# Optimization experiments

Measured on AMD Instinct MI355X. Metric: run time of the kernel, lower is better.

The kernel has to match this reference:

```python
import jax, jax.numpy as jnp
import numpy as np

DN = ('NHWC', 'HWIO', 'NHWC')
ITERS, LAM, MU = 100, 0.005, 1.0


def _psf_matrix():
    # Gaussian PSF mapping a 72x72 hi-res grid onto a 9x9 camera image -> (5184, 81)
    hi = (np.arange(72) + 0.5) * 9.0 / 72.0   # hi-res positions in lo-res pixel units
    lo = np.arange(9) + 0.5                   # lo-res pixel centers
    sig = 1.5                                 # sigma/px_size = 150/100
    g = np.exp(-(hi[:, None] - lo[None, :]) ** 2 / (2.0 * sig * sig))  # (72, 9)
    mat = np.einsum('ai,bj->abij', g, g).reshape(5184, 81)
    mat /= np.linalg.norm(mat, 2)  # spectral-normalize so the 1/mu gradient step converges
    return mat.astype(np.float32)


def _conv(x, w, b=None, stride=1, padding='VALID'):
    y = jax.lax.conv_general_dilated(x, w, (stride, stride), padding, dimension_numbers=DN)
    return y if b is None else y + b


def _convT(x, w):
    return jax.lax.conv_transpose(x, w, (3, 3), 'SAME', dimension_numbers=DN)


def _bn(x, g, b, eps=1e-3):
    m = jnp.mean(x, axis=(0, 1, 2), keepdims=True)
    v = jnp.var(x, axis=(0, 1, 2), keepdims=True)
    return g * (x - m) * jax.lax.rsqrt(v + eps) + b


def _maxpool(x, k):
    return jax.lax.reduce_window(x, -jnp.inf, jax.lax.max, (1, k, k, 1), (1, k, k, 1), 'SAME')


def _fista(x, mat):
    # x: (B,9,9,3) -> per-channel flatten (B,81,3); sparse code y: (B,5184,3)
    B = x.shape[0]
    im = x.reshape(B, 81, 3)
    y0 = jnp.zeros((B, 5184, 3), x.dtype)
    thr = LAM / MU

    def step(carry, _):
        y_tmp, y_last, t = carry
        proj = jnp.einsum('sm,bsc->bmc', mat, y_tmp)          # mat^T @ y
        re = jnp.einsum('sm,bmc->bsc', mat, im - proj)        # mat @ (im - mat^T y)
        w = y_tmp + re / MU
        y_new = jax.nn.relu(w - thr) - jax.nn.relu(-w - thr)  # soft threshold
        t_n = (1.0 + jnp.sqrt(1.0 + 4.0 * t * t)) / 2.0
        y_mom = y_new + (t - 1.0) / t_n * (y_new - y_last)    # momentum
        return (y_mom, y_new, t_n), None

    (_, y_final, _), _ = jax.lax.scan(step, (y0, y0, jnp.float32(1.0)), None, length=ITERS)
    return y_final  # (B, 5184, 3)


def _forward(x, mat, bn_x_g, bn_x_b, w5, b5, wx2, bx2, wy1, by1, wy7, by7,
             bn_y_g, bn_y_b, ww1, bw1, wd1, bnd1_g, bnd1_b, wd2, bnd2_g, bnd2_b,
             wu1, bnu1_g, bnu1_b, wu2):
    B = x.shape[0]
    # --- x path: compressed sensing -> inception conv branch ---
    xi = _fista(x, mat).reshape(B, 72, 72, 3)
    xi = jnp.pad(xi, ((0, 0), (1, 0), (1, 0), (0, 0)), mode='reflect')  # (B,73,73,3)
    xi = _bn(xi, bn_x_g, bn_x_b)
    xi = _conv(xi, w5, b5)                 # valid 5x5 -> (B,69,69,8)
    xi = _maxpool(xi, 4)                   # -> (B,18,18,8)
    xi = jax.nn.relu(_conv(xi, wx2, bx2))  # 1x1 -> (B,18,18,2)
    xi = _maxpool(xi, 2)                   # -> (B,9,9,2)
    # --- y path ---
    yi = jax.nn.relu(_conv(x, wy1, by1))
    yi = _conv(yi, wy7, by7, padding='SAME')
    yi = _bn(yi, bn_y_g, bn_y_b)           # (B,9,9,1)
    # --- w path ---
    wi = jax.nn.relu(_conv(x, ww1, bw1))   # (B,9,9,1)
    # --- z path: small U-net ---
    z1 = jax.nn.leaky_relu(_bn(_conv(x, wd1, stride=3, padding='SAME'), bnd1_g, bnd1_b), 0.2)   # (B,3,3,12)
    z2 = jax.nn.leaky_relu(_bn(_conv(z1, wd2, stride=3, padding='SAME'), bnd2_g, bnd2_b), 0.2)  # (B,1,1,24)
    z = jax.nn.relu(_bn(_convT(z2, wu1), bnu1_g, bnu1_b))  # (B,3,3,12)
    z = jnp.concatenate([z, z1], axis=-1)                  # (B,3,3,24)
    z = jax.nn.relu(_convT(z, wu2))                        # (B,9,9,1)
    return jnp.concatenate([wi, xi, yi, z], axis=-1)       # (B,9,9,5)


def setup_inputs() -> dict:
    key = jax.random.key(0)
    ks = jax.random.split(key, 12)
    n = jax.random.normal
    B = 64
    return {
        'x': jax.random.uniform(ks[0], (B, 9, 9, 3), jnp.float32),
        'mat': jnp.asarray(_psf_matrix()),
        'bn_x_g': jnp.ones(3), 'bn_x_b': jnp.zeros(3),
        'w5': n(ks[1], (5, 5, 3, 8)) * 0.1, 'b5': jnp.zeros(8),
        'wx2': n(ks[2], (1, 1, 8, 2)) * 0.1, 'bx2': jnp.zeros(2),
        'wy1': n(ks[3], (1, 1, 3, 1)) * 0.1, 'by1': jnp.zeros(1),
        'wy7': n(ks[4], (7, 7, 1, 1)) * 0.1, 'by7': jnp.zeros(1),
        'bn_y_g': jnp.ones(1), 'bn_y_b': jnp.zeros(1),
        'ww1': n(ks[5], (1, 1, 3, 1)) * 0.1, 'bw1': jnp.zeros(1),
        'wd1': n(ks[6], (3, 3, 3, 12)) * 0.1, 'bnd1_g': jnp.ones(12), 'bnd1_b': jnp.zeros(12),
        'wd2': n(ks[7], (3, 3, 12, 24)) * 0.1, 'bnd2_g': jnp.ones(24), 'bnd2_b': jnp.zeros(24),
        'wu1': n(ks[8], (3, 3, 24, 12)) * 0.1, 'bnu1_g': jnp.ones(12), 'bnu1_b': jnp.zeros(12),
        'wu2': n(ks[9], (3, 3, 24, 1)) * 0.1,
    }


def reference(x, mat, bn_x_g, bn_x_b, w5, b5, wx2, bx2, wy1, by1, wy7, by7,
              bn_y_g, bn_y_b, ww1, bw1, wd1, bnd1_g, bnd1_b, wd2, bnd2_g, bnd2_b,
              wu1, bnu1_g, bnu1_b, wu2):
    return _forward(x, mat, bn_x_g, bn_x_b, w5, b5, wx2, bx2, wy1, by1, wy7, by7,
                    bn_y_g, bn_y_b, ww1, bw1, wd1, bnd1_g, bnd1_b, wd2, bnd2_g, bnd2_b,
                    wu1, bnu1_g, bnu1_b, wu2)
```

## Files before the change

kernel.cpp:

```cpp
#include <hip/hip_runtime.h>
#include <hip/hip_bf16.h>
#include <math.h>

#define NS 5184

__device__ __forceinline__ float dpp_xor1_add(float v) {
  int s = __builtin_amdgcn_update_dpp(0, __float_as_int(v), 0xB1, 0xF, 0xF, true);
  return v + __int_as_float(s);
}
__device__ __forceinline__ float dpp_xor2_add(float v) {
  int s = __builtin_amdgcn_update_dpp(0, __float_as_int(v), 0x4E, 0xF, 0xF, true);
  return v + __int_as_float(s);
}

__global__ __launch_bounds__(576, 3) void cs_fista_small(
    const float* __restrict__ x, const float* __restrict__ mat,
    const float* __restrict__ wy1, const float* __restrict__ by1,
    const float* __restrict__ wy7, const float* __restrict__ by7,
    const float* __restrict__ bn_y_g, const float* __restrict__ bn_y_b,
    const float* __restrict__ ww1, const float* __restrict__ bw1,
    const float* __restrict__ wd1, const float* __restrict__ bnd1_g, const float* __restrict__ bnd1_b,
    const float* __restrict__ wd2, const float* __restrict__ bnd2_g, const float* __restrict__ bnd2_b,
    const float* __restrict__ wu1, const float* __restrict__ bnu1_g, const float* __restrict__ bnu1_b,
    const float* __restrict__ wu2,
    float* __restrict__ ws_y, float* __restrict__ bns, float* __restrict__ out)
{
  __shared__ __align__(16) float smem[16384];
  const int tid = threadIdx.x;
  const int blk = blockIdx.x;

  if (blk < 192) {
    const int bb = blk / 3, ch = blk % 3;
    float* GT  = smem;
    float* W1T = smem + 684;
    float* M9T = smem + 1368;
    float* IM  = smem + 1476;
    float* RED = smem + 1560;

    const int a    = tid >> 3;
    const int slot = tid & 7;
    const int b0   = slot * 9;

    for (int k = tid; k < 648; k += 576) {
      int aa = k / 9, i = k % 9;
      GT[i*76 + aa] = sqrtf(mat[aa*5913 + i*10]);
    }
    if (tid < 81) IM[tid] = x[(bb*81 + tid)*3 + ch];
    __syncthreads();

    float g_blk[9][9], g_row[9], gim[9];
    #pragma unroll
    for (int bl = 0; bl < 9; ++bl)
      #pragma unroll
      for (int j = 0; j < 9; ++j)
        g_blk[bl][j] = GT[j*76 + b0 + bl];
    #pragma unroll
    for (int i = 0; i < 9; ++i) g_row[i] = GT[i*76 + a];
    #pragma unroll
    for (int j = 0; j < 9; ++j) {
      float acc = 0.f;
      #pragma unroll
      for (int i = 0; i < 9; ++i) acc = fmaf(g_row[i], IM[i*9 + j], acc);
      gim[j] = acc;
    }
    float ym[9], yl[9];
    #pragma unroll
    for (int bl = 0; bl < 9; ++bl) { ym[bl] = 0.f; yl[bl] = 0.f; }
    const int lbase = (tid & 63) & 56;

    float t = 1.f;
    for (int it = 0; it < 100; ++it) {
      float pj[9];
      #pragma unroll
      for (int j = 0; j < 9; ++j) {
        float acc = 0.f;
        #pragma unroll
        for (int bl = 0; bl < 9; ++bl) acc = fmaf(ym[bl], g_blk[bl][j], acc);
        pj[j] = acc;
      }
      #pragma unroll
      for (int j = 0; j < 9; ++j) {
        pj[j] = dpp_xor1_add(pj[j]);
        pj[j] = dpp_xor2_add(pj[j]);
        pj[j] += __shfl_xor(pj[j], 4);
      }
      float sel = pj[0];
      sel = (slot == 1) ? pj[1] : sel;
      sel = (slot == 2) ? pj[2] : sel;
      sel = (slot == 3) ? pj[3] : sel;
      sel = (slot == 4) ? pj[4] : sel;
      sel = (slot == 5) ? pj[5] : sel;
      sel = (slot == 6) ? pj[6] : sel;
      sel = (slot == 7) ? pj[7] : sel;
      W1T[slot*76 + a] = sel;
      if (slot == 0) W1T[8*76 + a] = pj[8];
      __syncthreads();
      if (tid < 324) {
        int o = tid >> 2, sg = tid & 3;
        int i = o / 9, j = o - i*9;
        const float* gb = GT  + i*76;
        const float* wb = W1T + j*76;
        const float4* gr = (const float4*)(gb + sg*16);
        const float4* wr = (const float4*)(wb + sg*16);
        float4 g0 = gr[0], w0 = wr[0];
        float4 g1 = gr[1], w1 = wr[1];
        float4 g2 = gr[2], w2 = wr[2];
        float4 g3 = gr[3], w3 = wr[3];
        float p0 = g0.x*w0.x, p1 = g0.y*w0.y, p2 = g0.z*w0.z, p3 = g0.w*w0.w;
        p0 = fmaf(g1.x, w1.x, p0); p1 = fmaf(g1.y, w1.y, p1);
        p2 = fmaf(g1.z, w1.z, p2); p3 = fmaf(g1.w, w1.w, p3);
        p0 = fmaf(g2.x, w2.x, p0); p1 = fmaf(g2.y, w2.y, p1);
        p2 = fmaf(g2.z, w2.z, p2); p3 = fmaf(g2.w, w2.w, p3);
        p0 = fmaf(g3.x, w3.x, p0); p1 = fmaf(g3.y, w3.y, p1);
        p2 = fmaf(g3.z, w3.z, p2); p3 = fmaf(g3.w, w3.w, p3);
        if (sg == 0) {
          const float4* gt = (const float4*)(gb + 64);
          const float4* wt = (const float4*)(wb + 64);
          float4 g4 = gt[0], w4 = wt[0];
          float4 g5 = gt[1], w5 = wt[1];
          p0 = fmaf(g4.x, w4.x, p0); p1 = fmaf(g4.y, w4.y, p1);
          p2 = fmaf(g4.z, w4.z, p2); p3 = fmaf(g4.w, w4.w, p3);
          p0 = fmaf(g5.x, w5.x, p0); p1 = fmaf(g5.y, w5.y, p1);
          p2 = fmaf(g5.z, w5.z, p2); p3 = fmaf(g5.w, w5.w, p3);
        }
        float acc = (p0 + p1) + (p2 + p3);
        acc = dpp_xor1_add(acc);
        acc = dpp_xor2_add(acc);
        if (sg == 0) M9T[j*12 + i] = acc;
      }
      __syncthreads();
      const float tn  = 0.5f * (1.f + sqrtf(1.f + 4.f*t*t));
      const float mom = (t - 1.f) / tn;
      float gsel = gim[0];
      gsel = (slot == 1) ? gim[1] : gsel;
      gsel = (slot == 2) ? gim[2] : gsel;
      gsel = (slot == 3) ? gim[3] : gsel;
      gsel = (slot == 4) ? gim[4] : gsel;
      gsel = (slot == 5) ? gim[5] : gsel;
      gsel = (slot == 6) ? gim[6] : gsel;
      gsel = (slot == 7) ? gim[7] : gsel;
      float4 c0 = *(const float4*)(M9T + slot*12);
      float4 c1 = *(const float4*)(M9T + slot*12 + 4);
      float  c8 = M9T[slot*12 + 8];
      float tjs = gsel;
      tjs = fmaf(-g_row[0], c0.x, tjs);
      tjs = fmaf(-g_row[1], c0.y, tjs);
      tjs = fmaf(-g_row[2], c0.z, tjs);
      tjs = fmaf(-g_row[3], c0.w, tjs);
      tjs = fmaf(-g_row[4], c1.x, tjs);
      tjs = fmaf(-g_row[5], c1.y, tjs);
      tjs = fmaf(-g_row[6], c1.z, tjs);
      tjs = fmaf(-g_row[7], c1.w, tjs);
      tjs = fmaf(-g_row[8], c8,   tjs);
      float tj8 = 0.f;
      if (slot == 7) {
        float4 d0 = *(const float4*)(M9T + 96);
        float4 d1 = *(const float4*)(M9T + 100);
        float  d8 = M9T[104];
        tj8 = gim[8];
        tj8 = fmaf(-g_row[0], d0.x, tj8);
        tj8 = fmaf(-g_row[1], d0.y, tj8);
        tj8 = fmaf(-g_row[2], d0.z, tj8);
        tj8 = fmaf(-g_row[3], d0.w, tj8);
        tj8 = fmaf(-g_row[4], d1.x, tj8);
        tj8 = fmaf(-g_row[5], d1.y, tj8);
        tj8 = fmaf(-g_row[6], d1.z, tj8);
        tj8 = fmaf(-g_row[7], d1.w, tj8);
        tj8 = fmaf(-g_row[8], d8,   tj8);
      }
      float t2[9];
      t2[0] = __shfl(tjs, lbase + 0);
      t2[1] = __shfl(tjs, lbase + 1);
      t2[2] = __shfl(tjs, lbase + 2);
      t2[3] = __shfl(tjs, lbase + 3);
      t2[4] = __shfl(tjs, lbase + 4);
      t2[5] = __shfl(tjs, lbase + 5);
      t2[6] = __shfl(tjs, lbase + 6);
      t2[7] = __shfl(tjs, lbase + 7);
      t2[8] = __shfl(tj8, lbase + 7);
      #pragma unroll
      for (int bl = 0; bl < 9; ++bl) {
        float re = 0.f;
        #pragma unroll
        for (int j = 0; j < 9; ++j) re = fmaf(t2[j], g_blk[bl][j], re);
        float w  = ym[bl] + re;
        float yn = fmaxf(w - 0.005f, 0.f) - fmaxf(-w - 0.005f, 0.f);
        float y2 = fmaf(mom, yn - yl[bl], yn);
        yl[bl] = yn;
        ym[bl] = y2;
      }
      t = tn;
    }
    float* wp = ws_y + (bb*3 + ch)*NS + a*72 + b0;
    float wsum = 0.f, wss = 0.f;
    #pragma unroll
    for (int bl = 0; bl < 9; ++bl) {
      wp[bl] = yl[bl];
      float wt = (float)((1 + (a == 1)) * (1 + (b0 + bl == 1)));
      wsum = fmaf(wt, yl[bl], wsum);
      wss  = fmaf(wt * yl[bl], yl[bl], wss);
    }
    #pragma unroll
    for (int off = 32; off > 0; off >>= 1) {
      wsum += __shfl_down(wsum, off);
      wss  += __shfl_down(wss, off);
    }
    __syncthreads();
    if ((tid & 63) == 0) { RED[tid >> 6] = wsum; RED[16 + (tid >> 6)] = wss; }
    __syncthreads();
    if (tid == 0) {
      float s = 0.f, s2 = 0.f;
      for (int w = 0; w < 9; ++w) { s += RED[w]; s2 += RED[16 + w]; }
      atomicAdd(&bns[ch],     s);
      atomicAdd(&bns[3 + ch], s2);
    }
  } else {
    float* TY  = smem;
    float* Y7  = smem + 5184;
    float* Z1  = smem;
    float* Z2  = smem + 6912;
    float* ZU  = smem + 8448;
    float* RED = smem + 15360;

    const float vwy10 = wy1[0], vwy11 = wy1[1], vwy12 = wy1[2], vby1 = by1[0];
    const float vww10 = ww1[0], vww11 = ww1[1], vww12 = ww1[2], vbw1 = bw1[0];
    for (int k = tid; k < NS; k += 576) {
      const float* xp = x + 3*k;
      float x0 = xp[0], x1 = xp[1], x2 = xp[2];
      out[5*k] = fmaxf(fmaf(x2, vww12, fmaf(x1, vww11, fmaf(x0, vww10, vbw1))), 0.f);
      TY[k]    = fmaxf(fmaf(x2, vwy12, fmaf(x1, vwy11, fmaf(x0, vwy10, vby1))), 0.f);
    }
    __syncthreads();
    float ps = 0.f, pss = 0.f;
    const float vby7 = by7[0];
    for (int k = tid; k < NS; k += 576) {
      int bb = k / 81, p = k % 81, h = p / 9, w = p % 9;
      float acc = vby7;
      for (int kh = 0; kh < 7; ++kh) {
        int hh = h + kh - 3;
        if (hh < 0 || hh > 8) continue;
        for (int kw = 0; kw < 7; ++kw) {
          int wi = w + kw - 3;
          if (wi < 0 || wi > 8) continue;
          acc = fmaf(TY[bb*81 + hh*9 + wi], wy7[kh*7 + kw], acc);
        }
      }
      Y7[k] = acc;
      ps += acc; pss += acc*acc;
    }
    #pragma unroll
    for (int off = 32; off > 0; off >>= 1) {
      ps  += __shfl_down(ps, off);
      pss += __shfl_down(pss, off);
    }
    if ((tid & 63) == 0) { RED[tid >> 6] = ps; RED[16 + (tid >> 6)] = pss; }
    __syncthreads();
    if (tid == 0) {
      float s = 0.f, s2 = 0.f;
      for (int w = 0; w < 9; ++w) { s += RED[w]; s2 += RED[16 + w]; }
      float m  = s  * (1.f/5184.f);
      float v  = s2 * (1.f/5184.f) - m*m;
      float sc = bn_y_g[0] * rsqrtf(v + 1e-3f);
      RED[32] = sc;
      RED[33] = bn_y_b[0] - m*sc;
    }
    __syncthreads();
    {
      float sc = RED[32], sh = RED[33];
      for (int k = tid; k < NS; k += 576) out[5*k + 3] = fmaf(Y7[k], sc, sh);
    }
    __syncthreads();
    if (tid < 128) RED[tid] = 0.f;
    __syncthreads();
    for (int k = tid; k < 6912; k += 576) {
      int bb = k / 108, r = k % 108, u = r / 36, v3 = (r / 12) % 3, oc = r % 12;
      float acc = 0.f;
      #pragma unroll
      for (int kh = 0; kh < 3; ++kh)
        #pragma unroll
        for (int kw = 0; kw < 3; ++kw) {
          const float* xp = x + (bb*81 + (3*u + kh)*9 + (3*v3 + kw))*3;
          #pragma unroll
          for (int cc = 0; cc < 3; ++cc)
            acc = fmaf(xp[cc], wd1[((kh*3 + kw)*3 + cc)*12 + oc], acc);
        }
      Z1[k] = acc;
    }
    __syncthreads();
    for (int k = tid; k < 6912; k += 576) {
      float v = Z1[k]; int oc = k % 12;
      atomicAdd(&RED[oc], v); atomicAdd(&RED[64 + oc], v*v);
    }
    __syncthreads();
    for (int k = tid; k < 6912; k += 576) {
      int oc = k % 12;
      float m  = RED[oc] * (1.f/576.f);
      float v  = RED[64 + oc] * (1.f/576.f) - m*m;
      float sc = bnd1_g[oc] * rsqrtf(v + 1e-3f);
      float z  = fmaf(Z1[k] - m, sc, bnd1_b[oc]);
      Z1[k] = z >= 0.f ? z : 0.2f*z;
    }
    __syncthreads();
    if (tid < 128) RED[tid] = 0.f;
    __syncthreads();
    for (int k = tid; k < 1536; k += 576) {
      int bb = k / 24, oc = k % 24;
      float acc = 0.f;
      for (int q = 0; q < 9; ++q)
        #pragma unroll
        for (int ic = 0; ic < 12; ++ic)
          acc = fmaf(Z1[bb*108 + q*12 + ic], wd2[(q*12 + ic)*24 + oc], acc);
      Z2[k] = acc;
    }
    __syncthreads();
    for (int k = tid; k < 1536; k += 576) {
      float v = Z2[k]; int oc = k % 24;
      atomicAdd(&RED[oc], v); atomicAdd(&RED[64 + oc], v*v);
    }
    __syncthreads();
    for (int k = tid; k < 1536; k += 576) {
      int oc = k % 24;
      float m  = RED[oc] * (1.f/64.f);
      float v  = RED[64 + oc] * (1.f/64.f) - m*m;
      float sc = bnd2_g[oc] * rsqrtf(v + 1e-3f);
      float z  = fmaf(Z2[k] - m, sc, bnd2_b[oc]);
      Z2[k] = z >= 0.f ? z : 0.2f*z;
    }
    __syncthreads();
    if (tid < 128) RED[tid] = 0.f;
    __syncthreads();
    for (int k = tid; k < 6912; k += 576) {
      int bb = k / 108, r = k % 108, yy = r / 36, xx = (r / 12) % 3, o = r % 12;
      const float* wpq = wu1 + ((2 - yy)*3 + (2 - xx))*288 + o;
      const float* zp = Z2 + bb*24;
      float acc = 0.f;
      #pragma unroll
      for (int i = 0; i < 24; ++i) acc = fmaf(zp[i], wpq[i*12], acc);
      ZU[k] = acc;
    }
    __syncthreads();
    for (int k = tid; k < 6912; k += 576) {
      float v = ZU[k]; int o = k % 12;
      atomicAdd(&RED[o], v); atomicAdd(&RED[64 + o], v*v);
    }
    __syncthreads();
    for (int k = tid; k < 6912; k += 576) {
      int o = k % 12;
      float m  = RED[o] * (1.f/576.f);
      float v  = RED[64 + o] * (1.f/576.f) - m*m;
      float sc = bnu1_g[o] * rsqrtf(v + 1e-3f);
      float z  = fmaf(ZU[k] - m, sc, bnu1_b[o]);
      ZU[k] = fmaxf(z, 0.f);
    }
    __syncthreads();
    for (int k = tid; k < NS; k += 576) {
      int bb = k / 81, p = k % 81, h = p / 9, w = p % 9;
      int u = h / 3, v3 = w / 3, kh = 2 - (h % 3), kw = 2 - (w % 3);
      const float* wpp = wu2 + (kh*3 + kw)*24;
      const float* zu = ZU + bb*108 + u*36 + v3*12;
      const float* z1 = Z1 + bb*108 + u*36 + v3*12;
      float acc = 0.f;
      #pragma unroll
      for (int i = 0; i < 12; ++i) acc = fmaf(zu[i], wpp[i], acc);
      #pragma unroll
      for (int i = 0; i < 12; ++i) acc = fmaf(z1[i], wpp[12 + i], acc);
      out[5*k + 4] = fmaxf(acc, 0.f);
    }
  }
}

__global__ __launch_bounds__(384) void cs_xpath(
    const float* __restrict__ ws_y, const float* __restrict__ bns,
    const float* __restrict__ bn_x_g, const float* __restrict__ bn_x_b,
    const float* __restrict__ w5, const float* __restrict__ b5,
    const float* __restrict__ wx2, const float* __restrict__ bx2,
    float* __restrict__ out)
{
  __shared__ __align__(16) float xin[3*5256 + 600];
  float* w5s = xin + 3*5256;
  const int tid = threadIdx.x, bb = blockIdx.x;

  const float N = 64.f * 73.f * 73.f;
  float sc[3], sh[3];
  #pragma unroll
  for (int c = 0; c < 3; ++c) {
    float m = bns[c]/N;
    float v = bns[3 + c]/N - m*m;
    sc[c] = bn_x_g[c]*rsqrtf(v + 1e-3f);
    sh[c] = bn_x_b[c] - m*sc[c];
  }
  #pragma unroll
  for (int c = 0; c < 3; ++c) {
    const float* src = ws_y + (bb*3 + c)*NS;
    float* dst = xin + c*5256;
    float s1 = sc[c], s2 = sh[c];
    for (int k = tid; k < NS; k += 384) {
      int h = k / 72, w = k - h*72;
      dst[h*73 + w] = fmaf(src[k], s1, s2);
    }
  }
  for (int k = tid; k < 600; k += 384) w5s[k] = w5[k];
  float b5r[8];
  #pragma unroll
  for (int o = 0; o < 8; ++o) b5r[o] = b5[o];
  __syncthreads();

  float mx[8];
  const bool active = tid < 324;
  if (active) {
    int p = tid / 18, q = tid % 18;
    #pragma unroll
    for (int o = 0; o < 8; ++o) mx[o] = -1e30f;
    int r0 = 4*p - 1; if (r0 < 0) r0 = 0;
    int r1 = 4*p + 2; if (r1 > 68) r1 = 68;
    int c0 = 4*q - 1; if (c0 < 0) c0 = 0;
    int c1 = 4*q + 2; if (c1 > 68) c1 = 68;
    for (int r = r0; r <= r1; ++r) {
      for (int cc = c0; cc <= c1; ++cc) {
        float acc[8];
        #pragma unroll
        for (int o = 0; o < 8; ++o) acc[o] = b5r[o];
        #pragma unroll 1
        for (int kh = 0; kh < 5; ++kh) {
          int hs = r + kh - 1; hs = hs < 0 ? -hs : hs;
          int rowb = hs*73;
          #pragma unroll 1
          for (int kw = 0; kw < 5; ++kw) {
            int wsc = cc + kw - 1; wsc = wsc < 0 ? -wsc : wsc;
            const float* wp = &w5s[(kh*5 + kw)*24];
            int aI = rowb + wsc;
            float x0 = xin[aI], x1 = xin[5256 + aI], x2 = xin[2*5256 + aI];
            #pragma unroll
            for (int o = 0; o < 8; ++o) {
              float t = fmaf(x0, wp[o], acc[o]);
              t = fmaf(x1, wp[8 + o], t);
              acc[o] = fmaf(x2, wp[16 + o], t);
            }
          }
        }
        #pragma unroll
        for (int o = 0; o < 8; ++o) mx[o] = fmaxf(mx[o], acc[o]);
      }
    }
  }
  __syncthreads();
  float* pool = xin;
  if (active) {
    int p = tid / 18, q = tid % 18;
    #pragma unroll
    for (int o = 0; o < 8; ++o) pool[(p*18 + q)*8 + o] = mx[o];
  }
  __syncthreads();
  if (tid < 162) {
    int u = tid & 1, pix = tid >> 1;
    int h = pix / 9, w = pix % 9;
    float m = -1e30f;
    #pragma unroll
    for (int dp = 0; dp < 2; ++dp)
      #pragma unroll
      for (int dq = 0; dq < 2; ++dq) {
        int p = 2*h + dp, q = 2*w + dq;
        float acc = bx2[u];
        #pragma unroll
        for (int o = 0; o < 8; ++o) acc = fmaf(pool[(p*18 + q)*8 + o], wx2[o*2 + u], acc);
        m = fmaxf(m, fmaxf(acc, 0.f));
      }
    out[(bb*81 + pix)*5 + 1 + u] = m;
  }
}

extern "C" void kernel_launch(void* const* d_in, const int* in_sizes, int n_in,
                              void* d_out, int out_size, void* d_ws, size_t ws_size,
                              hipStream_t stream) {
  (void)in_sizes; (void)n_in; (void)out_size; (void)ws_size;
  const float* x      = (const float*)d_in[0];
  const float* mat    = (const float*)d_in[1];
  const float* bn_x_g = (const float*)d_in[2];
  const float* bn_x_b = (const float*)d_in[3];
  const float* w5     = (const float*)d_in[4];
  const float* b5     = (const float*)d_in[5];
  const float* wx2    = (const float*)d_in[6];
  const float* bx2    = (const float*)d_in[7];
  const float* wy1    = (const float*)d_in[8];
  const float* by1    = (const float*)d_in[9];
  const float* wy7    = (const float*)d_in[10];
  const float* by7    = (const float*)d_in[11];
  const float* bn_y_g = (const float*)d_in[12];
  const float* bn_y_b = (const float*)d_in[13];
  const float* ww1    = (const float*)d_in[14];
  const float* bw1    = (const float*)d_in[15];
  const float* wd1    = (const float*)d_in[16];
  const float* bnd1_g = (const float*)d_in[17];
  const float* bnd1_b = (const float*)d_in[18];
  const float* wd2    = (const float*)d_in[19];
  const float* bnd2_g = (const float*)d_in[20];
  const float* bnd2_b = (const float*)d_in[21];
  const float* wu1    = (const float*)d_in[22];
  const float* bnu1_g = (const float*)d_in[23];
  const float* bnu1_b = (const float*)d_in[24];
  const float* wu2    = (const float*)d_in[25];

  float* outp = (float*)d_out;
  float* ws_y = (float*)d_ws;
  float* bns  = ws_y + 64*3*5184;

  hipMemsetAsync(bns, 0, 6*sizeof(float), stream);
  cs_fista_small<<<dim3(193), dim3(576), 0, stream>>>(
      x, mat, wy1, by1, wy7, by7, bn_y_g, bn_y_b, ww1, bw1,
      wd1, bnd1_g, bnd1_b, wd2, bnd2_g, bnd2_b, wu1, bnu1_g, bnu1_b, wu2,
      ws_y, bns, outp);
  cs_xpath<<<dim3(64), dim3(384), 0, stream>>>(
      ws_y, bns, bn_x_g, bn_x_b, w5, b5, wx2, bx2, outp);
}
```

Measured before the change: 250.4 us.

## Split xpath conv into row bands across more blocks and stream PSF factors from LDS

The x-path conv+pool kernel now launches three row-band blocks per image, each with 512 threads, so each pooling cell is shared by four threads and the results are combined with shuffles. This smaller LDS tile allows higher occupancy and more parallelism than the 64-block launch. The FISTA kernel no longer keeps the 81-register g_blk array and instead reads separable PSF rows from a new LDS array as float4 vectors, which cuts register pressure at the cost of extra LDS traffic each iteration. The loop-invariant gsel selection is also hoisted out of the iteration loop.

```diff
diff --git a/kernel.cpp b/kernel.cpp
--- a/kernel.cpp
+++ b/kernel.cpp
@@ -36,6 +36,7 @@
     float* M9T = smem + 1368;
     float* IM  = smem + 1476;
     float* RED = smem + 1560;
+    float* GR  = smem + 1600;
 
     const int a    = tid >> 3;
     const int slot = tid & 7;
@@ -43,17 +44,14 @@
 
     for (int k = tid; k < 648; k += 576) {
       int aa = k / 9, i = k % 9;
-      GT[i*76 + aa] = sqrtf(mat[aa*5913 + i*10]);
+      float v = sqrtf(mat[aa*5913 + i*10]);
+      GT[i*76 + aa] = v;
+      GR[aa*12 + i] = v;
     }
     if (tid < 81) IM[tid] = x[(bb*81 + tid)*3 + ch];
     __syncthreads();
 
-    float g_blk[9][9], g_row[9], gim[9];
-    #pragma unroll
-    for (int bl = 0; bl < 9; ++bl)
-      #pragma unroll
-      for (int j = 0; j < 9; ++j)
-        g_blk[bl][j] = GT[j*76 + b0 + bl];
+    float g_row[9], gim[9];
     #pragma unroll
     for (int i = 0; i < 9; ++i) g_row[i] = GT[i*76 + a];
     #pragma unroll
@@ -63,6 +61,14 @@
       for (int i = 0; i < 9; ++i) acc = fmaf(g_row[i], IM[i*9 + j], acc);
       gim[j] = acc;
     }
+    float gsel = gim[0];
+    gsel = (slot == 1) ? gim[1] : gsel;
+    gsel = (slot == 2) ? gim[2] : gsel;
+    gsel = (slot == 3) ? gim[3] : gsel;
+    gsel = (slot == 4) ? gim[4] : gsel;
+    gsel = (slot == 5) ? gim[5] : gsel;
+    gsel = (slot == 6) ? gim[6] : gsel;
+    gsel = (slot == 7) ? gim[7] : gsel;
     float ym[9], yl[9];
     #pragma unroll
     for (int bl = 0; bl < 9; ++bl) { ym[bl] = 0.f; yl[bl] = 0.f; }
@@ -72,11 +78,22 @@
     for (int it = 0; it < 100; ++it) {
       float pj[9];
       #pragma unroll
-      for (int j = 0; j < 9; ++j) {
-        float acc = 0.f;
-        #pragma unroll
-        for (int bl = 0; bl < 9; ++bl) acc = fmaf(ym[bl], g_blk[bl][j], acc);
-        pj[j] = acc;
+      for (int j = 0; j < 9; ++j) pj[j] = 0.f;
+      #pragma unroll
+      for (int bl = 0; bl < 9; ++bl) {
+        const float4* gr4 = (const float4*)(GR + (b0 + bl)*12);
+        float4 q0 = gr4[0], q1 = gr4[1];
+        float  q8 = GR[(b0 + bl)*12 + 8];
+        float  yb = ym[bl];
+        pj[0] = fmaf(yb, q0.x, pj[0]);
+        pj[1] = fmaf(yb, q0.y, pj[1]);
+        pj[2] = fmaf(yb, q0.z, pj[2]);
+        pj[3] = fmaf(yb, q0.w, pj[3]);
+        pj[4] = fmaf(yb, q1.x, pj[4]);
+        pj[5] = fmaf(yb, q1.y, pj[5]);
+        pj[6] = fmaf(yb, q1.z, pj[6]);
+        pj[7] = fmaf(yb, q1.w, pj[7]);
+        pj[8] = fmaf(yb, q8,   pj[8]);
       }
       #pragma unroll
       for (int j = 0; j < 9; ++j) {
@@ -131,14 +148,6 @@
       __syncthreads();
       const float tn  = 0.5f * (1.f + sqrtf(1.f + 4.f*t*t));
       const float mom = (t - 1.f) / tn;
-      float gsel = gim[0];
-      gsel = (slot == 1) ? gim[1] : gsel;
-      gsel = (slot == 2) ? gim[2] : gsel;
-      gsel = (slot == 3) ? gim[3] : gsel;
-      gsel = (slot == 4) ? gim[4] : gsel;
-      gsel = (slot == 5) ? gim[5] : gsel;
-      gsel = (slot == 6) ? gim[6] : gsel;
-      gsel = (slot == 7) ? gim[7] : gsel;
       float4 c0 = *(const float4*)(M9T + slot*12);
       float4 c1 = *(const float4*)(M9T + slot*12 + 4);
       float  c8 = M9T[slot*12 + 8];
@@ -180,9 +189,18 @@
       t2[8] = __shfl(tj8, lbase + 7);
       #pragma unroll
       for (int bl = 0; bl < 9; ++bl) {
-        float re = 0.f;
-        #pragma unroll
-        for (int j = 0; j < 9; ++j) re = fmaf(t2[j], g_blk[bl][j], re);
+        const float4* gr4 = (const float4*)(GR + (b0 + bl)*12);
+        float4 q0 = gr4[0], q1 = gr4[1];
+        float  q8 = GR[(b0 + bl)*12 + 8];
+        float re = t2[0]*q0.x;
+        re = fmaf(t2[1], q0.y, re);
+        re = fmaf(t2[2], q0.z, re);
+        re = fmaf(t2[3], q0.w, re);
+        re = fmaf(t2[4], q1.x, re);
+        re = fmaf(t2[5], q1.y, re);
+        re = fmaf(t2[6], q1.z, re);
+        re = fmaf(t2[7], q1.w, re);
+        re = fmaf(t2[8], q8,   re);
         float w  = ym[bl] + re;
         float yn = fmaxf(w - 0.005f, 0.f) - fmaxf(-w - 0.005f, 0.f);
         float y2 = fmaf(mom, yn - yl[bl], yn);
@@ -369,16 +387,20 @@
   }
 }
 
-__global__ __launch_bounds__(384) void cs_xpath(
+__global__ __launch_bounds__(512) void cs_xpath(
     const float* __restrict__ ws_y, const float* __restrict__ bns,
     const float* __restrict__ bn_x_g, const float* __restrict__ bn_x_b,
     const float* __restrict__ w5, const float* __restrict__ b5,
     const float* __restrict__ wx2, const float* __restrict__ bx2,
     float* __restrict__ out)
 {
-  __shared__ __align__(16) float xin[3*5256 + 600];
-  float* w5s = xin + 3*5256;
-  const int tid = threadIdx.x, bb = blockIdx.x;
+  __shared__ __align__(16) float xin[3*2044];
+  __shared__ __align__(16) float w5s[600];
+  __shared__ float pool[108*8];
+  const int tid = threadIdx.x;
+  const int img = blockIdx.x / 3, band = blockIdx.x % 3;
+  const int lo    = (band == 0) ? 0 : (band == 1 ? 22 : 46);
+  const int nrows = (band == 1) ? 28 : 26;
 
   const float N = 64.f * 73.f * 73.f;
   float sc[3], sh[3];
@@ -389,53 +411,71 @@
     sc[c] = bn_x_g[c]*rsqrtf(v + 1e-3f);
     sh[c] = bn_x_b[c] - m*sc[c];
   }
+  const int nstage = nrows * 72;
   #pragma unroll
   for (int c = 0; c < 3; ++c) {
-    const float* src = ws_y + (bb*3 + c)*NS;
-    float* dst = xin + c*5256;
+    const float* src = ws_y + (img*3 + c)*NS + lo*72;
+    float* dst = xin + c*2044;
     float s1 = sc[c], s2 = sh[c];
-    for (int k = tid; k < NS; k += 384) {
+    for (int k = tid; k < nstage; k += 512) {
       int h = k / 72, w = k - h*72;
       dst[h*73 + w] = fmaf(src[k], s1, s2);
     }
   }
-  for (int k = tid; k < 600; k += 384) w5s[k] = w5[k];
+  for (int k = tid; k < 600; k += 512) w5s[k] = w5[k];
   float b5r[8];
   #pragma unroll
   for (int o = 0; o < 8; ++o) b5r[o] = b5[o];
   __syncthreads();
 
+  const int cell = tid >> 2, t4 = tid & 3;
   float mx[8];
-  const bool active = tid < 324;
-  if (active) {
-    int p = tid / 18, q = tid % 18;
-    #pragma unroll
-    for (int o = 0; o < 8; ++o) mx[o] = -1e30f;
+  #pragma unroll
+  for (int o = 0; o < 8; ++o) mx[o] = -1e30f;
+  if (cell < 108) {
+    int prl = cell / 18, pc = cell % 18;
+    int p = 6*band + prl;
     int r0 = 4*p - 1; if (r0 < 0) r0 = 0;
     int r1 = 4*p + 2; if (r1 > 68) r1 = 68;
-    int c0 = 4*q - 1; if (c0 < 0) c0 = 0;
-    int c1 = 4*q + 2; if (c1 > 68) c1 = 68;
-    for (int r = r0; r <= r1; ++r) {
-      for (int cc = c0; cc <= c1; ++cc) {
+    int c0 = 4*pc - 1; if (c0 < 0) c0 = 0;
+    int c1 = 4*pc + 2; if (c1 > 68) c1 = 68;
+    int nc = c1 - c0 + 1;
+    int cnt = (r1 - r0 + 1) * nc;
+    #pragma unroll
+    for (int k4 = 0; k4 < 4; ++k4) {
+      int idx = t4 + 4*k4;
+      if (idx < cnt) {
+        int rr = idx / nc;
+        int r  = r0 + rr;
+        int cc = c0 + idx - rr*nc;
         float acc[8];
         #pragma unroll
         for (int o = 0; o < 8; ++o) acc[o] = b5r[o];
-        #pragma unroll 1
+        #pragma unroll
         for (int kh = 0; kh < 5; ++kh) {
           int hs = r + kh - 1; hs = hs < 0 ? -hs : hs;
-          int rowb = hs*73;
-          #pragma unroll 1
+          int rowb = (hs - lo)*73;
+          #pragma unroll
           for (int kw = 0; kw < 5; ++kw) {
             int wsc = cc + kw - 1; wsc = wsc < 0 ? -wsc : wsc;
-            const float* wp = &w5s[(kh*5 + kw)*24];
+            const float4* wq = (const float4*)(w5s + (kh*5 + kw)*24);
+            float4 wa0 = wq[0], wa1 = wq[1];
+            float4 wb0 = wq[2], wb1 = wq[3];
+            float4 wc0 = wq[4], wc1 = wq[5];
             int aI = rowb + wsc;
-            float x0 = xin[aI], x1 = xin[5256 + aI], x2 = xin[2*5256 + aI];
-            #pragma unroll
-            for (int o = 0; o < 8; ++o) {
-              float t = fmaf(x0, wp[o], acc[o]);
-              t = fmaf(x1, wp[8 + o], t);
-              acc[o] = fmaf(x2, wp[16 + o], t);
-            }
+            float x0 = xin[aI], x1 = xin[2044 + aI], x2 = xin[2*2044 + aI];
+            acc[0] = fmaf(x0, wa0.x, acc[0]); acc[1] = fmaf(x0, wa0.y, acc[1]);
+            acc[2] = fmaf(x0, wa0.z, acc[2]); acc[3] = fmaf(x0, wa0.w, acc[3]);
+            acc[4] = fmaf(x0, wa1.x, acc[4]); acc[5] = fmaf(x0, wa1.y, acc[5]);
+            acc[6] = fmaf(x0, wa1.z, acc[6]); acc[7] = fmaf(x0, wa1.w, acc[7]);
+            acc[0] = fmaf(x1, wb0.x, acc[0]); acc[1] = fmaf(x1, wb0.y, acc[1]);
+            acc[2] = fmaf(x1, wb0.z, acc[2]); acc[3] = fmaf(x1, wb0.w, acc[3]);
+            acc[4] = fmaf(x1, wb1.x, acc[4]); acc[5] = fmaf(x1, wb1.y, acc[5]);
+            acc[6] = fmaf(x1, wb1.z, acc[6]); acc[7] = fmaf(x1, wb1.w, acc[7]);
+            acc[0] = fmaf(x2, wc0.x, acc[0]); acc[1] = fmaf(x2, wc0.y, acc[1]);
+            acc[2] = fmaf(x2, wc0.z, acc[2]); acc[3] = fmaf(x2, wc0.w, acc[3]);
+            acc[4] = fmaf(x2, wc1.x, acc[4]); acc[5] = fmaf(x2, wc1.y, acc[5]);
+            acc[6] = fmaf(x2, wc1.z, acc[6]); acc[7] = fmaf(x2, wc1.w, acc[7]);
           }
         }
         #pragma unroll
@@ -443,29 +483,31 @@
       }
     }
   }
+  #pragma unroll
+  for (int o = 0; o < 8; ++o) {
+    mx[o] = fmaxf(mx[o], __shfl_xor(mx[o], 1));
+    mx[o] = fmaxf(mx[o], __shfl_xor(mx[o], 2));
+  }
+  if (cell < 108 && t4 == 0) {
+    #pragma unroll
+    for (int o = 0; o < 8; ++o) pool[cell*8 + o] = mx[o];
+  }
   __syncthreads();
-  float* pool = xin;
-  if (active) {
-    int p = tid / 18, q = tid % 18;
-    #pragma unroll
-    for (int o = 0; o < 8; ++o) pool[(p*18 + q)*8 + o] = mx[o];
-  }
-  __syncthreads();
-  if (tid < 162) {
+  if (tid < 54) {
     int u = tid & 1, pix = tid >> 1;
-    int h = pix / 9, w = pix % 9;
+    int ohl = pix / 9, ow = pix % 9;
     float m = -1e30f;
     #pragma unroll
     for (int dp = 0; dp < 2; ++dp)
       #pragma unroll
       for (int dq = 0; dq < 2; ++dq) {
-        int p = 2*h + dp, q = 2*w + dq;
+        int cl = (2*ohl + dp)*18 + (2*ow + dq);
         float acc = bx2[u];
         #pragma unroll
-        for (int o = 0; o < 8; ++o) acc = fmaf(pool[(p*18 + q)*8 + o], wx2[o*2 + u], acc);
+        for (int o = 0; o < 8; ++o) acc = fmaf(pool[cl*8 + o], wx2[o*2 + u], acc);
         m = fmaxf(m, fmaxf(acc, 0.f));
       }
-    out[(bb*81 + pix)*5 + 1 + u] = m;
+    out[(img*81 + (3*band + ohl)*9 + ow)*5 + 1 + u] = m;
   }
 }
 
@@ -509,6 +551,6 @@
       x, mat, wy1, by1, wy7, by7, bn_y_g, bn_y_b, ww1, bw1,
       wd1, bnd1_g, bnd1_b, wd2, bnd2_g, bnd2_b, wu1, bnu1_g, bnu1_b, wu2,
       ws_y, bns, outp);
-  cs_xpath<<<dim3(64), dim3(384), 0, stream>>>(
+  cs_xpath<<<dim3(192), dim3(512), 0, stream>>>(
       ws_y, bns, bn_x_g, bn_x_b, w5, b5, wx2, bx2, outp);
 }
```

After: 242.8 us. 1.03x faster.
